# Kernel tuning notes

Hardware: AMD Instinct MI355X
Metric: run time of the kernel (lower is better)

## Reference

```python
import jax, jax.numpy as jnp
import numpy as np

N = 100000      # nodes
E = 1600000     # directed edges
F_IN = 128      # input features
H = 64          # hidden_channels
C = 32          # num_classes


def setup_inputs() -> dict:
    key = jax.random.key(0)
    ks = jax.random.split(key, 8)
    x = jax.random.normal(ks[0], (N, F_IN), jnp.float32)
    edge_index = jax.random.randint(ks[1], (2, E), 0, N, jnp.int32)
    W1 = jax.random.normal(ks[2], (F_IN, H), jnp.float32) * (1.0 / np.sqrt(F_IN))
    b1 = jnp.zeros((H,), jnp.float32)
    W2 = jax.random.normal(ks[3], (H, H), jnp.float32) * (1.0 / np.sqrt(H))
    b2 = jnp.zeros((H,), jnp.float32)
    Wout = jax.random.normal(ks[4], (H, C), jnp.float32) * (1.0 / np.sqrt(H))
    bout = jnp.zeros((C,), jnp.float32)
    return {"x": x, "edge_index": edge_index, "W1": W1, "b1": b1,
            "W2": W2, "b2": b2, "Wout": Wout, "bout": bout}


def gcn_conv(x, W, b, src, dst, n):
    """PyG GCNConv: out = D^-1/2 (A + I) D^-1/2 (X W) + b,
    with degree computed on A + I."""
    h = x @ W  # [N, out]
    ones = jnp.ones(dst.shape[0], h.dtype)
    deg = jax.ops.segment_sum(ones, dst, num_segments=n) + 1.0  # self-loop
    dinv = jax.lax.rsqrt(deg)                                   # [N]
    coef = dinv[src] * dinv[dst]                                # [E]
    agg = jax.ops.segment_sum(h[src] * coef[:, None], dst, num_segments=n)
    agg = agg + h * (dinv * dinv)[:, None]                      # self-loop message
    return agg + b


def reference(x, edge_index, W1, b1, W2, b2, Wout, bout):
    src, dst = edge_index[0], edge_index[1]
    n = x.shape[0]
    h = jax.nn.relu(gcn_conv(x, W1, b1, src, dst, n))
    # dropout(p=0.5) is a no-op in eval mode
    h = jax.nn.relu(gcn_conv(h, W2, b2, src, dst, n))
    return jax.nn.softmax(h @ Wout + bout, axis=1)
```

## Files before the change

### kernel.cpp

```cpp
#include <hip/hip_runtime.h>
#include <stdint.h>


typedef unsigned short u16;
typedef unsigned int u32;
typedef unsigned long long u64t;
typedef __attribute__((ext_vector_type(8))) short bf16x8;
typedef __attribute__((ext_vector_type(4))) float f32x4;
typedef __attribute__((ext_vector_type(2))) float f32x2;

#define GN 100000
#define GE 1600000
#define NBKT 196
#define BCAP 10240
#define EBLK 782
#define B24 16777216
#define QSC 1048576.0f
#define QIV 9.5367431640625e-7f

__device__ __forceinline__ float bf2f(u32 lo16) {
  union { u32 i; float f; } v; v.i = lo16 << 16; return v.f;
}
__device__ __forceinline__ u16 f2bf(float f) {
  union { float f; u32 i; } v; v.f = f;
  u32 x = v.i;
  u32 r = x + 0x7fffu + ((x >> 16) & 1u);
  return (u16)(r >> 16);
}
__device__ __forceinline__ u32 pack2(float a, float b) {
  return (u32)f2bf(a) | ((u32)f2bf(b) << 16);
}
__device__ __forceinline__ f32x2 unpk(u32 u) {
  union { u32 i; float f; } lo, hi;
  lo.i = u << 16; hi.i = u & 0xffff0000u;
  return (f32x2){lo.f, hi.f};
}

__global__ __launch_bounds__(256) void k_detect(const u16* __restrict__ xs,
                                                int* __restrict__ flag,
                                                int* __restrict__ ccount) {
  __shared__ int cnt;
  if (threadIdx.x == 0) cnt = 0;
  if (threadIdx.x < NBKT) ccount[threadIdx.x] = 0;
  __syncthreads();
  int w = 0;
#pragma unroll
  for (int i = 0; i < 16; i++) {
    int s = threadIdx.x * 16 + i;
    u32 u = xs[(size_t)s * 1562];
    u32 ex = (u >> 7) & 0xffu;
    if (ex == 0xffu || ex < 0x40u) w++;
  }
  atomicAdd(&cnt, w);
  __syncthreads();
  if (threadIdx.x == 0) flag[0] = (cnt >= 64) ? 0 : 1;
}

__global__ __launch_bounds__(256) void k_partA(const int* __restrict__ src,
                                               const int* __restrict__ dst,
                                               int* __restrict__ ccount, int E,
                                               const void* p2, const void* p3,
                                               const void* p4, const void* p5,
                                               const void* p6, const void* p7,
                                               const int* __restrict__ flag,
                                               float* __restrict__ Wf,
                                               u16* __restrict__ Wb1,
                                               u16* __restrict__ Wb2,
                                               u16* __restrict__ Wbo,
                                               u32* __restrict__ pairs) {
  int tid = threadIdx.x;
  if (blockIdx.x >= EBLK) {
    int i = (blockIdx.x - EBLK) * 256 + tid;
    bool isbf = flag[0] != 0;
    if (i < 14496) {
      const void* sp; int off;
      if (i < 8192)       { sp = p2; off = i; }
      else if (i < 8256)  { sp = p3; off = i - 8192; }
      else if (i < 12352) { sp = p4; off = i - 8256; }
      else if (i < 12416) { sp = p5; off = i - 12352; }
      else if (i < 14464) { sp = p6; off = i - 12416; }
      else                { sp = p7; off = i - 14464; }
      Wf[i] = isbf ? bf2f((u32)((const u16*)sp)[off]) : ((const float*)sp)[off];
    } else if (i < 14496 + 12288) {
      int idx = i - 14496;
      const void* W; u16* dstp;
      if (idx < 8192) { W = p2; dstp = Wb1; }
      else            { W = p4; dstp = Wb2; idx -= 8192; }
      int j  = idx & 7;
      int l  = (idx >> 3) & 63;
      int c  = (idx >> 9) & 3;
      int kc = idx >> 11;
      int k = kc * 32 + (l >> 4) * 8 + j;
      int n = c * 16 + (l & 15);
      dstp[idx] = isbf ? ((const u16*)W)[k * 64 + n]
                       : f2bf(((const float*)W)[k * 64 + n]);
    } else if (i < 14496 + 12288 + 2048) {
      int idx = i - 14496 - 12288;
      int j  = idx & 7;
      int l  = (idx >> 3) & 63;
      int c  = (idx >> 9) & 1;
      int kc = idx >> 10;
      int k = kc * 32 + (l >> 4) * 8 + j;
      int n = c * 16 + (l & 15);
      Wbo[idx] = isbf ? ((const u16*)p6)[k * 32 + n]
                      : f2bf(((const float*)p6)[k * 32 + n]);
    }
    return;
  }
  __shared__ int hist[256];
  __shared__ int boff[256];
  __shared__ int fill[256];
  __shared__ int gbase[256];
  __shared__ int sc[256];
  __shared__ u32 buf[2048];
  __shared__ int adr[2048];
  __shared__ int stotal;
  hist[tid] = 0;
  __syncthreads();
  int e0 = (blockIdx.x * 256 + tid) * 8;
  int s_[8], d_[8];
  int cnt = 0;
  if (e0 + 8 <= E) {
    const int4* sp = (const int4*)(src + e0);
    const int4* dp = (const int4*)(dst + e0);
#pragma unroll
    for (int q = 0; q < 2; q++) {
      int4 sv = sp[q], dv = dp[q];
      s_[4 * q + 0] = sv.x; s_[4 * q + 1] = sv.y;
      s_[4 * q + 2] = sv.z; s_[4 * q + 3] = sv.w;
      d_[4 * q + 0] = dv.x; d_[4 * q + 1] = dv.y;
      d_[4 * q + 2] = dv.z; d_[4 * q + 3] = dv.w;
    }
    cnt = 8;
  } else {
    for (int q = 0; q < 8 && e0 + q < E; q++) {
      s_[q] = src[e0 + q]; d_[q] = dst[e0 + q]; cnt++;
    }
  }
  for (int q = 0; q < cnt; q++) atomicAdd(&hist[d_[q] >> 9], 1);
  __syncthreads();
  int v = hist[tid];
  sc[tid] = v;
  __syncthreads();
#pragma unroll
  for (int off = 1; off < 256; off <<= 1) {
    int a = (tid >= off) ? sc[tid - off] : 0;
    __syncthreads();
    sc[tid] += a;
    __syncthreads();
  }
  int excl = sc[tid] - v;
  boff[tid] = excl;
  fill[tid] = excl;
  if (tid == 255) stotal = sc[255];
  if (tid < NBKT && v > 0) gbase[tid] = tid * BCAP + atomicAdd(&ccount[tid], v);
  __syncthreads();
  for (int q = 0; q < cnt; q++) {
    int bkt = d_[q] >> 9;
    int p = atomicAdd(&fill[bkt], 1);
    buf[p] = ((u32)s_[q] << 9) | ((u32)d_[q] & 511u);
    adr[p] = gbase[bkt] + (p - boff[bkt]);
  }
  __syncthreads();
  int total = stotal;
  for (int j = tid; j < total; j += 256) pairs[adr[j]] = buf[j];
}

__global__ __launch_bounds__(256) void k_partBdlo(u32* __restrict__ pairs,
                                                  const int* __restrict__ ccount,
                                                  int* __restrict__ deg, int N) {
  __shared__ u32 P[BCAP];
  __shared__ u32 S[BCAP];
  __shared__ int cnt[512];
  __shared__ int sc[256];
  int b = blockIdx.x, tid = threadIdx.x;
  int beg = b * BCAP, m = ccount[b];
  if (m > BCAP) m = BCAP;
  cnt[tid] = 0; cnt[tid + 256] = 0;
  for (int i = tid; i < m; i += 256) P[i] = pairs[beg + i];
  __syncthreads();
  for (int i = tid; i < m; i += 256) atomicAdd(&cnt[P[i] & 511u], 1);
  __syncthreads();
  int c0 = cnt[2 * tid], c1 = cnt[2 * tid + 1];
  int s = c0 + c1;
  sc[tid] = s;
  __syncthreads();
#pragma unroll
  for (int off = 1; off < 256; off <<= 1) {
    int a = (tid >= off) ? sc[tid - off] : 0;
    __syncthreads();
    sc[tid] += a;
    __syncthreads();
  }
  int excl = sc[tid] - s;
  cnt[2 * tid] = excl;
  cnt[2 * tid + 1] = excl + c0;
  int n0 = (b << 9) + 2 * tid, n1 = n0 + 1;
  if (n0 < N) deg[n0] = c0;
  if (n1 < N) deg[n1] = c1;
  __syncthreads();
  for (int i = tid; i < m; i += 256) {
    u32 p = P[i];
    int pos = atomicAdd(&cnt[p & 511u], 1);
    S[pos] = p;
  }
  __syncthreads();
  for (int i = tid; i < m; i += 256) pairs[beg + i] = S[i];
}

template <int K, int XMODE>
__global__ __launch_bounds__(256) void k_mgemm(const void* __restrict__ X,
                                               const u16* __restrict__ Wb,
                                               const int* __restrict__ deg,
                                               const int* __restrict__ flag,
                                               u16* __restrict__ out, int M) {
  constexpr int NKC = K / 32;
  constexpr int P = K + 8;
  __shared__ u16 Bs[NKC * 4 * 64 * 8];
  __shared__ u16 As[128 * P];
  int tid = threadIdx.x;
  bool isbf = (XMODE == 1) ? true : (flag[0] != 0);
#pragma unroll
  for (int i = 0; i < NKC; i++)
    ((uint4*)Bs)[i * 256 + tid] = ((const uint4*)Wb)[i * 256 + tid];

  int rowbase = blockIdx.x * 128;
  int rowsValid = M - rowbase; if (rowsValid > 128) rowsValid = 128;
  if (isbf) {
    constexpr int F8 = K / 8;
    constexpr int NL = K / 16;
    const uint4* Xg = (const uint4*)X;
    uint4 v[NL];
#pragma unroll
    for (int i = 0; i < NL; i++) {
      int q = i * 256 + tid;
      int row = q / F8, c8 = q % F8;
      v[i] = (row < rowsValid) ? Xg[(size_t)(rowbase + row) * F8 + c8]
                               : make_uint4(0, 0, 0, 0);
    }
#pragma unroll
    for (int i = 0; i < NL; i++) {
      int q = i * 256 + tid;
      int row = q / F8, c8 = q % F8;
      *(uint4*)&As[row * P + c8 * 8] = v[i];
    }
  } else {
    constexpr int F4 = K / 4;
    constexpr int NL = K / 8;
    const float4* Xg = (const float4*)X;
    float4 v[NL];
#pragma unroll
    for (int i = 0; i < NL; i++) {
      int q = i * 256 + tid;
      int row = q / F4, c4 = q % F4;
      v[i] = (row < rowsValid) ? Xg[(size_t)(rowbase + row) * F4 + c4]
                               : make_float4(0.f, 0.f, 0.f, 0.f);
    }
#pragma unroll
    for (int i = 0; i < NL; i++) {
      int q = i * 256 + tid;
      int row = q / F4, c4 = q % F4;
      u32* d = (u32*)&As[row * P + c4 * 4];
      d[0] = pack2(v[i].x, v[i].y);
      d[1] = pack2(v[i].z, v[i].w);
    }
  }
  __syncthreads();

  int lane = tid & 63, wave = tid >> 6;
  int m0 = lane & 15;
  int koff = (lane >> 4) * 8;
  f32x4 acc[2][4];
#pragma unroll
  for (int t = 0; t < 2; t++)
#pragma unroll
    for (int c = 0; c < 4; c++) acc[t][c] = (f32x4){0.f, 0.f, 0.f, 0.f};

#pragma unroll
  for (int kc = 0; kc < NKC; kc++) {
    union { uint4 v; bf16x8 s; } a[2];
#pragma unroll
    for (int t = 0; t < 2; t++) {
      int rl = wave * 32 + t * 16 + m0;
      a[t].v = *(const uint4*)&As[rl * P + kc * 32 + koff];
    }
#pragma unroll
    for (int c = 0; c < 4; c++) {
      bf16x8 b = *(const bf16x8*)&Bs[((kc * 4 + c) * 64 + lane) * 8];
      acc[0][c] = __builtin_amdgcn_mfma_f32_16x16x32_bf16(a[0].s, b, acc[0][c], 0, 0, 0);
      acc[1][c] = __builtin_amdgcn_mfma_f32_16x16x32_bf16(a[1].s, b, acc[1][c], 0, 0, 0);
    }
  }
  __syncthreads();
  int cl = lane & 15, rq = (lane >> 4) * 4;
#pragma unroll
  for (int t = 0; t < 2; t++)
#pragma unroll
    for (int reg = 0; reg < 4; reg++) {
      int rl = wave * 32 + t * 16 + rq + reg;
      int r = rowbase + rl;
      float s = (r < M) ? rsqrtf((float)deg[r] + 1.0f) : 0.f;
#pragma unroll
      for (int c = 0; c < 4; c++)
        As[rl * P + c * 16 + cl] = f2bf(acc[t][c][reg] * s);
    }
  __syncthreads();
  uint4* outg = (uint4*)out;
#pragma unroll
  for (int i = 0; i < 4; i++) {
    int q = i * 256 + tid;
    int row = q >> 3, c8 = q & 7;
    int r = rowbase + row;
    if (r < M) outg[(size_t)r * 8 + c8] = *(uint4*)&As[row * P + c8 * 8];
  }
}

template <int MODE>
__global__ __launch_bounds__(1024) void k_aggr(const u16* __restrict__ g,
                                               const u32* __restrict__ pairs,
                                               const int* __restrict__ ccount,
                                               const float* __restrict__ bias,
                                               const u16* __restrict__ Wfrag,
                                               const float* __restrict__ bof,
                                               const int* __restrict__ flag,
                                               void* __restrict__ outv) {
  __shared__ __align__(16) u64t accU[512 * 33];
  __shared__ int cntE[512];
  u16* T16 = (u16*)accU;
  int tid = threadIdx.x;
  int b = blockIdx.x;
  for (int i = tid; i < 512 * 33; i += 1024) accU[i] = 0ull;
  if (tid < 512) cntE[tid] = 0;
  __syncthreads();

  int beg = b * BCAP;
  int m = ccount[b];
  if (m > BCAP) m = BCAP;
  int end = beg + m;
  int o = tid >> 3, fq = tid & 7;
  const uint4* gp4 = (const uint4*)g;

  int C = (m + 127) >> 7;
  int lo = beg + o * C;
  int hi = lo + C; if (hi > end) hi = end;

  f32x2 a0 = {0.f, 0.f}, a1 = {0.f, 0.f}, a2 = {0.f, 0.f}, a3 = {0.f, 0.f};
  int cur = 0, runN = 0;

#define FLUSH()                                                              \
  do {                                                                       \
    if (runN > 0) {                                                          \
      int nb_ = runN * B24;                                                  \
      u64t* rp_ = &accU[cur * 33 + fq * 4];                                  \
      int q0_ = (int)(a0.x * QSC) + nb_;                                     \
      int q1_ = (int)(a0.y * QSC) + nb_;                                     \
      int q2_ = (int)(a1.x * QSC) + nb_;                                     \
      int q3_ = (int)(a1.y * QSC) + nb_;                                     \
      int q4_ = (int)(a2.x * QSC) + nb_;                                     \
      int q5_ = (int)(a2.y * QSC) + nb_;                                     \
      int q6_ = (int)(a3.x * QSC) + nb_;                                     \
      int q7_ = (int)(a3.y * QSC) + nb_;                                     \
      atomicAdd(rp_ + 0, ((u64t)(u32)q0_) | (((u64t)(u32)q1_) << 32));       \
      atomicAdd(rp_ + 1, ((u64t)(u32)q2_) | (((u64t)(u32)q3_) << 32));       \
      atomicAdd(rp_ + 2, ((u64t)(u32)q4_) | (((u64t)(u32)q5_) << 32));       \
      atomicAdd(rp_ + 3, ((u64t)(u32)q6_) | (((u64t)(u32)q7_) << 32));       \
      if (fq == 0) atomicAdd(&cntE[cur], runN);                              \
      a0 = (f32x2){0.f, 0.f}; a1 = (f32x2){0.f, 0.f};                        \
      a2 = (f32x2){0.f, 0.f}; a3 = (f32x2){0.f, 0.f};                        \
      runN = 0;                                                              \
    }                                                                        \
  } while (0)

#define STEP(p_, v_)                                                         \
  do {                                                                       \
    int d_ = (int)((p_) & 511u);                                             \
    if (d_ != cur) { FLUSH(); cur = d_; }                                    \
    a0 += unpk((v_).x); a1 += unpk((v_).y);                                  \
    a2 += unpk((v_).z); a3 += unpk((v_).w);                                  \
    runN++;                                                                  \
  } while (0)

  for (int e = lo; e < hi; e += 4) {
    int n4 = hi - e;
    u32 p0 = pairs[e];
    u32 p1 = pairs[(n4 > 1) ? e + 1 : e];
    u32 p2 = pairs[(n4 > 2) ? e + 2 : e];
    u32 p3 = pairs[(n4 > 3) ? e + 3 : e];
    uint4 v0 = gp4[(size_t)(p0 >> 9) * 8 + fq];
    uint4 v1 = gp4[(size_t)(p1 >> 9) * 8 + fq];
    uint4 v2 = gp4[(size_t)(p2 >> 9) * 8 + fq];
    uint4 v3 = gp4[(size_t)(p3 >> 9) * 8 + fq];
    STEP(p0, v0);
    if (n4 > 1) STEP(p1, v1);
    if (n4 > 2) STEP(p2, v2);
    if (n4 > 3) STEP(p3, v3);
  }
  FLUSH();
#undef STEP
#undef FLUSH
  __syncthreads();

  u32 pk[4][4];
  int rowq[4], c8q[4];
#pragma unroll
  for (int i = 0; i < 4; i++) {
    int q = i * 1024 + tid;
    int row = q >> 3, c8 = q & 7;
    rowq[i] = row; c8q[i] = c8;
    int node = b * 512 + row;
    float f0 = 0.f, f1 = 0.f, f2 = 0.f, f3 = 0.f;
    float f4 = 0.f, f5 = 0.f, f6 = 0.f, f7 = 0.f;
    if (node < GN) {
      uint4 sv = gp4[(size_t)node * 8 + c8];
      int n = cntE[row];
      int nb = n * B24;
      float dv = rsqrtf((float)n + 1.0f);
      float4 b0 = ((const float4*)bias)[c8 * 2];
      float4 b1 = ((const float4*)bias)[c8 * 2 + 1];
      const u64t* up = &accU[row * 33 + c8 * 4];
      u64t w0 = up[0], w1 = up[1], w2 = up[2], w3 = up[3];
      int a0i = (int)((u32)w0) - nb, a1i = (int)((u32)(w0 >> 32)) - nb;
      int a2i = (int)((u32)w1) - nb, a3i = (int)((u32)(w1 >> 32)) - nb;
      int a4i = (int)((u32)w2) - nb, a5i = (int)((u32)(w2 >> 32)) - nb;
      int a6i = (int)((u32)w3) - nb, a7i = (int)((u32)(w3 >> 32)) - nb;
      f0 = fmaxf(dv * ((float)a0i * QIV + bf2f(sv.x & 0xffffu)) + b0.x, 0.f);
      f1 = fmaxf(dv * ((float)a1i * QIV + bf2f(sv.x >> 16))     + b0.y, 0.f);
      f2 = fmaxf(dv * ((float)a2i * QIV + bf2f(sv.y & 0xffffu)) + b0.z, 0.f);
      f3 = fmaxf(dv * ((float)a3i * QIV + bf2f(sv.y >> 16))     + b0.w, 0.f);
      f4 = fmaxf(dv * ((float)a4i * QIV + bf2f(sv.z & 0xffffu)) + b1.x, 0.f);
      f5 = fmaxf(dv * ((float)a5i * QIV + bf2f(sv.z >> 16))     + b1.y, 0.f);
      f6 = fmaxf(dv * ((float)a6i * QIV + bf2f(sv.w & 0xffffu)) + b1.z, 0.f);
      f7 = fmaxf(dv * ((float)a7i * QIV + bf2f(sv.w >> 16))     + b1.w, 0.f);
    }
    pk[i][0] = pack2(f0, f1); pk[i][1] = pack2(f2, f3);
    pk[i][2] = pack2(f4, f5); pk[i][3] = pack2(f6, f7);
  }
  __syncthreads();
#pragma unroll
  for (int i = 0; i < 4; i++)
    *(uint4*)&T16[rowq[i] * 72 + c8q[i] * 8] =
        make_uint4(pk[i][0], pk[i][1], pk[i][2], pk[i][3]);
  __syncthreads();

  int lane = tid & 63, wave = tid >> 6;
  int m0 = lane & 15, koff = (lane >> 4) * 8;
  int cl = lane & 15, rq = (lane >> 4) * 4;
  if (MODE == 0) {
    bf16x8 bfr[2][4];
#pragma unroll
    for (int kc = 0; kc < 2; kc++)
#pragma unroll
      for (int c = 0; c < 4; c++)
        bfr[kc][c] = *(const bf16x8*)&Wfrag[((kc * 4 + c) * 64 + lane) * 8];
    f32x4 acc[2][4];
#pragma unroll
    for (int t = 0; t < 2; t++)
#pragma unroll
      for (int c = 0; c < 4; c++) acc[t][c] = (f32x4){0.f, 0.f, 0.f, 0.f};
#pragma unroll
    for (int kc = 0; kc < 2; kc++) {
      union { uint4 v; bf16x8 s; } a[2];
#pragma unroll
      for (int t = 0; t < 2; t++)
        a[t].v = *(const uint4*)&T16[(wave * 32 + t * 16 + m0) * 72 + kc * 32 + koff];
#pragma unroll
      for (int c = 0; c < 4; c++) {
        acc[0][c] = __builtin_amdgcn_mfma_f32_16x16x32_bf16(a[0].s, bfr[kc][c], acc[0][c], 0, 0, 0);
        acc[1][c] = __builtin_amdgcn_mfma_f32_16x16x32_bf16(a[1].s, bfr[kc][c], acc[1][c], 0, 0, 0);
      }
    }
    __syncthreads();
#pragma unroll
    for (int t = 0; t < 2; t++)
#pragma unroll
      for (int reg = 0; reg < 4; reg++) {
        int rl = wave * 32 + t * 16 + rq + reg;
        int node = b * 512 + rl;
        float s = (node < GN) ? rsqrtf((float)cntE[rl] + 1.0f) : 0.f;
#pragma unroll
        for (int c = 0; c < 4; c++)
          T16[rl * 72 + c * 16 + cl] = f2bf(acc[t][c][reg] * s);
      }
    __syncthreads();
    uint4* og = (uint4*)outv;
#pragma unroll
    for (int i = 0; i < 4; i++) {
      int q = i * 1024 + tid;
      int row = q >> 3, c8 = q & 7;
      int node = b * 512 + row;
      if (node < GN) og[(size_t)node * 8 + c8] = *(uint4*)&T16[row * 72 + c8 * 8];
    }
  } else {
    bf16x8 bfr[2][2];
#pragma unroll
    for (int kc = 0; kc < 2; kc++)
#pragma unroll
      for (int cc = 0; cc < 2; cc++)
        bfr[kc][cc] = *(const bf16x8*)&Wfrag[((kc * 2 + cc) * 64 + lane) * 8];
    f32x4 acc[2][2];
#pragma unroll
    for (int t = 0; t < 2; t++)
#pragma unroll
      for (int c = 0; c < 2; c++) acc[t][c] = (f32x4){0.f, 0.f, 0.f, 0.f};
#pragma unroll
    for (int kc = 0; kc < 2; kc++) {
      union { uint4 v; bf16x8 s; } a[2];
#pragma unroll
      for (int t = 0; t < 2; t++)
        a[t].v = *(const uint4*)&T16[(wave * 32 + t * 16 + m0) * 72 + kc * 32 + koff];
#pragma unroll
      for (int c = 0; c < 2; c++) {
        acc[0][c] = __builtin_amdgcn_mfma_f32_16x16x32_bf16(a[0].s, bfr[kc][c], acc[0][c], 0, 0, 0);
        acc[1][c] = __builtin_amdgcn_mfma_f32_16x16x32_bf16(a[1].s, bfr[kc][c], acc[1][c], 0, 0, 0);
      }
    }
    bool isbf = flag[0] != 0;
    float bb0 = bof[cl], bb1 = bof[16 + cl];
#pragma unroll
    for (int t = 0; t < 2; t++)
#pragma unroll
      for (int reg = 0; reg < 4; reg++) {
        int r = b * 512 + wave * 32 + t * 16 + rq + reg;
        float v0 = acc[t][0][reg] + bb0;
        float v1 = acc[t][1][reg] + bb1;
        float mx = fmaxf(v0, v1);
        mx = fmaxf(mx, __shfl_xor(mx, 1));
        mx = fmaxf(mx, __shfl_xor(mx, 2));
        mx = fmaxf(mx, __shfl_xor(mx, 4));
        mx = fmaxf(mx, __shfl_xor(mx, 8));
        float e0 = __expf(v0 - mx), e1 = __expf(v1 - mx);
        float s = e0 + e1;
        s += __shfl_xor(s, 1);
        s += __shfl_xor(s, 2);
        s += __shfl_xor(s, 4);
        s += __shfl_xor(s, 8);
        float inv = 1.f / s;
        if (r < GN) {
          if (isbf) {
            u16* go = (u16*)outv;
            go[(size_t)r * 32 + cl]      = f2bf(e0 * inv);
            go[(size_t)r * 32 + 16 + cl] = f2bf(e1 * inv);
          } else {
            float* go = (float*)outv;
            go[(size_t)r * 32 + cl]      = e0 * inv;
            go[(size_t)r * 32 + 16 + cl] = e1 * inv;
          }
        }
      }
  }
}

extern "C" void kernel_launch(void* const* d_in, const int* in_sizes, int n_in,
                              void* d_out, int out_size, void* d_ws, size_t ws_size,
                              hipStream_t stream) {
  (void)in_sizes; (void)n_in; (void)out_size; (void)ws_size;
  const void* x  = d_in[0];
  const int* ei  = (const int*)d_in[1];
  const int E = GE;
  const int* srcI = ei;
  const int* dstI = ei + E;

  char* ws = (char*)d_ws;
  int*   flag   = (int*)(ws + 0);
  int*   ccount = (int*)(ws + 256);
  int*   deg    = (int*)(ws + 4096);
  float* Wf     = (float*)(ws + 404480);
  u16*   Wb1    = (u16*)(ws + 462464);
  u16*   Wb2    = (u16*)(ws + 478848);
  u16*   Wbo    = (u16*)(ws + 487040);
  u32*   pairs  = (u32*)(ws + 491520);
  u16*   gA     = (u16*)(ws + 8519680);
  u16*   gB     = (u16*)(ws + 21319680);

  float* b1f = Wf + 8192;
  float* b2f = Wf + 12352;
  float* bof = Wf + 14464;

  k_detect<<<1, 256, 0, stream>>>((const u16*)x, flag, ccount);
  k_partA<<<EBLK + 113, 256, 0, stream>>>(srcI, dstI, ccount, E,
                                          d_in[2], d_in[3], d_in[4], d_in[5],
                                          d_in[6], d_in[7], flag,
                                          Wf, Wb1, Wb2, Wbo, pairs);
  k_partBdlo<<<NBKT, 256, 0, stream>>>(pairs, ccount, deg, GN);
  k_mgemm<128, 0><<<782, 256, 0, stream>>>(x, Wb1, deg, flag, gA, GN);
  k_aggr<0><<<NBKT, 1024, 0, stream>>>(gA, pairs, ccount, b1f, Wb2, bof, flag, gB);
  k_aggr<1><<<NBKT, 1024, 0, stream>>>(gB, pairs, ccount, b2f, Wbo, bof, flag, d_out);
}
```

Before: 227.3 us.

## Halve destination bucket size to 256 nodes to double aggregation blocks

Nodes are now bucketed in groups of 256 instead of 512 destinations, which gives 391 buckets instead of 196. The partition, local sort, degree and aggregation kernels are reworked to match: 8-bit destination packing, smaller shared-memory arrays, and one 16-row MFMA tile per wave instead of two. The goal is to fill all compute units during the aggregation kernels, since 196 blocks cannot occupy the whole GPU. In exchange there are more blocks with fewer edges each, a tighter per-bucket capacity margin, and a higher occupancy hint on the 1024-thread kernel.

```diff
diff --git a/kernel.cpp b/kernel.cpp
--- a/kernel.cpp
+++ b/kernel.cpp
@@ -11,8 +11,8 @@
 
 #define GN 100000
 #define GE 1600000
-#define NBKT 196
-#define BCAP 10240
+#define NB2 391
+#define BC2 5120
 #define EBLK 782
 #define B24 16777216
 #define QSC 1048576.0f
@@ -40,20 +40,21 @@
                                                 int* __restrict__ flag,
                                                 int* __restrict__ ccount) {
   __shared__ int cnt;
-  if (threadIdx.x == 0) cnt = 0;
-  if (threadIdx.x < NBKT) ccount[threadIdx.x] = 0;
+  int tid = threadIdx.x;
+  if (tid == 0) cnt = 0;
+  for (int i = tid; i < NB2; i += 256) ccount[i] = 0;
   __syncthreads();
   int w = 0;
 #pragma unroll
   for (int i = 0; i < 16; i++) {
-    int s = threadIdx.x * 16 + i;
+    int s = tid * 16 + i;
     u32 u = xs[(size_t)s * 1562];
     u32 ex = (u >> 7) & 0xffu;
     if (ex == 0xffu || ex < 0x40u) w++;
   }
   atomicAdd(&cnt, w);
   __syncthreads();
-  if (threadIdx.x == 0) flag[0] = (cnt >= 64) ? 0 : 1;
+  if (tid == 0) flag[0] = (cnt >= 64) ? 0 : 1;
 }
 
 __global__ __launch_bounds__(256) void k_partA(const int* __restrict__ src,
@@ -107,15 +108,15 @@
     }
     return;
   }
-  __shared__ int hist[256];
-  __shared__ int boff[256];
-  __shared__ int fill[256];
-  __shared__ int gbase[256];
+  __shared__ int hist[512];
+  __shared__ int boff[512];
+  __shared__ int fill[512];
+  __shared__ int gbase[512];
   __shared__ int sc[256];
   __shared__ u32 buf[2048];
   __shared__ int adr[2048];
   __shared__ int stotal;
-  hist[tid] = 0;
+  hist[tid] = 0; hist[tid + 256] = 0;
   __syncthreads();
   int e0 = (blockIdx.x * 256 + tid) * 8;
   int s_[8], d_[8];
@@ -137,10 +138,11 @@
       s_[q] = src[e0 + q]; d_[q] = dst[e0 + q]; cnt++;
     }
   }
-  for (int q = 0; q < cnt; q++) atomicAdd(&hist[d_[q] >> 9], 1);
-  __syncthreads();
-  int v = hist[tid];
-  sc[tid] = v;
+  for (int q = 0; q < cnt; q++) atomicAdd(&hist[d_[q] >> 8], 1);
+  __syncthreads();
+  int c0 = hist[2 * tid], c1 = hist[2 * tid + 1];
+  int s = c0 + c1;
+  sc[tid] = s;
   __syncthreads();
 #pragma unroll
   for (int off = 1; off < 256; off <<= 1) {
@@ -149,16 +151,17 @@
     sc[tid] += a;
     __syncthreads();
   }
-  int excl = sc[tid] - v;
-  boff[tid] = excl;
-  fill[tid] = excl;
+  int excl = sc[tid] - s;
+  boff[2 * tid] = excl;       boff[2 * tid + 1] = excl + c0;
+  fill[2 * tid] = excl;       fill[2 * tid + 1] = excl + c0;
   if (tid == 255) stotal = sc[255];
-  if (tid < NBKT && v > 0) gbase[tid] = tid * BCAP + atomicAdd(&ccount[tid], v);
+  if (c0 > 0) gbase[2 * tid]     = (2 * tid) * BC2 + atomicAdd(&ccount[2 * tid], c0);
+  if (c1 > 0) gbase[2 * tid + 1] = (2 * tid + 1) * BC2 + atomicAdd(&ccount[2 * tid + 1], c1);
   __syncthreads();
   for (int q = 0; q < cnt; q++) {
-    int bkt = d_[q] >> 9;
+    int bkt = d_[q] >> 8;
     int p = atomicAdd(&fill[bkt], 1);
-    buf[p] = ((u32)s_[q] << 9) | ((u32)d_[q] & 511u);
+    buf[p] = ((u32)s_[q] << 8) | ((u32)d_[q] & 255u);
     adr[p] = gbase[bkt] + (p - boff[bkt]);
   }
   __syncthreads();
@@ -169,21 +172,20 @@
 __global__ __launch_bounds__(256) void k_partBdlo(u32* __restrict__ pairs,
                                                   const int* __restrict__ ccount,
                                                   int* __restrict__ deg, int N) {
-  __shared__ u32 P[BCAP];
-  __shared__ u32 S[BCAP];
-  __shared__ int cnt[512];
+  __shared__ u32 P[BC2];
+  __shared__ u32 S[BC2];
+  __shared__ int cnt[256];
   __shared__ int sc[256];
   int b = blockIdx.x, tid = threadIdx.x;
-  int beg = b * BCAP, m = ccount[b];
-  if (m > BCAP) m = BCAP;
-  cnt[tid] = 0; cnt[tid + 256] = 0;
+  int beg = b * BC2, m = ccount[b];
+  if (m > BC2) m = BC2;
+  cnt[tid] = 0;
   for (int i = tid; i < m; i += 256) P[i] = pairs[beg + i];
   __syncthreads();
-  for (int i = tid; i < m; i += 256) atomicAdd(&cnt[P[i] & 511u], 1);
-  __syncthreads();
-  int c0 = cnt[2 * tid], c1 = cnt[2 * tid + 1];
-  int s = c0 + c1;
-  sc[tid] = s;
+  for (int i = tid; i < m; i += 256) atomicAdd(&cnt[P[i] & 255u], 1);
+  __syncthreads();
+  int v = cnt[tid];
+  sc[tid] = v;
   __syncthreads();
 #pragma unroll
   for (int off = 1; off < 256; off <<= 1) {
@@ -192,16 +194,14 @@
     sc[tid] += a;
     __syncthreads();
   }
-  int excl = sc[tid] - s;
-  cnt[2 * tid] = excl;
-  cnt[2 * tid + 1] = excl + c0;
-  int n0 = (b << 9) + 2 * tid, n1 = n0 + 1;
-  if (n0 < N) deg[n0] = c0;
-  if (n1 < N) deg[n1] = c1;
+  int excl = sc[tid] - v;
+  int n0 = (b << 8) + tid;
+  if (n0 < N) deg[n0] = v;
+  cnt[tid] = excl;
   __syncthreads();
   for (int i = tid; i < m; i += 256) {
     u32 p = P[i];
-    int pos = atomicAdd(&cnt[p & 511u], 1);
+    int pos = atomicAdd(&cnt[p & 255u], 1);
     S[pos] = p;
   }
   __syncthreads();
@@ -316,26 +316,26 @@
 }
 
 template <int MODE>
-__global__ __launch_bounds__(1024) void k_aggr(const u16* __restrict__ g,
-                                               const u32* __restrict__ pairs,
-                                               const int* __restrict__ ccount,
-                                               const float* __restrict__ bias,
-                                               const u16* __restrict__ Wfrag,
-                                               const float* __restrict__ bof,
-                                               const int* __restrict__ flag,
-                                               void* __restrict__ outv) {
-  __shared__ __align__(16) u64t accU[512 * 33];
-  __shared__ int cntE[512];
+__global__ __launch_bounds__(1024, 8) void k_aggr(const u16* __restrict__ g,
+                                                  const u32* __restrict__ pairs,
+                                                  const int* __restrict__ ccount,
+                                                  const float* __restrict__ bias,
+                                                  const u16* __restrict__ Wfrag,
+                                                  const float* __restrict__ bof,
+                                                  const int* __restrict__ flag,
+                                                  void* __restrict__ outv) {
+  __shared__ __align__(16) u64t accU[256 * 33];
+  __shared__ int cntE[256];
   u16* T16 = (u16*)accU;
   int tid = threadIdx.x;
   int b = blockIdx.x;
-  for (int i = tid; i < 512 * 33; i += 1024) accU[i] = 0ull;
-  if (tid < 512) cntE[tid] = 0;
-  __syncthreads();
-
-  int beg = b * BCAP;
+  for (int i = tid; i < 256 * 33; i += 1024) accU[i] = 0ull;
+  if (tid < 256) cntE[tid] = 0;
+  __syncthreads();
+
+  int beg = b * BC2;
   int m = ccount[b];
-  if (m > BCAP) m = BCAP;
+  if (m > BC2) m = BC2;
   int end = beg + m;
   int o = tid >> 3, fq = tid & 7;
   const uint4* gp4 = (const uint4*)g;
@@ -373,7 +373,7 @@
 
 #define STEP(p_, v_)                                                         \
   do {                                                                       \
-    int d_ = (int)((p_) & 511u);                                             \
+    int d_ = (int)((p_) & 255u);                                             \
     if (d_ != cur) { FLUSH(); cur = d_; }                                    \
     a0 += unpk((v_).x); a1 += unpk((v_).y);                                  \
     a2 += unpk((v_).z); a3 += unpk((v_).w);                                  \
@@ -386,10 +386,10 @@
     u32 p1 = pairs[(n4 > 1) ? e + 1 : e];
     u32 p2 = pairs[(n4 > 2) ? e + 2 : e];
     u32 p3 = pairs[(n4 > 3) ? e + 3 : e];
-    uint4 v0 = gp4[(size_t)(p0 >> 9) * 8 + fq];
-    uint4 v1 = gp4[(size_t)(p1 >> 9) * 8 + fq];
-    uint4 v2 = gp4[(size_t)(p2 >> 9) * 8 + fq];
-    uint4 v3 = gp4[(size_t)(p3 >> 9) * 8 + fq];
+    uint4 v0 = gp4[(size_t)(p0 >> 8) * 8 + fq];
+    uint4 v1 = gp4[(size_t)(p1 >> 8) * 8 + fq];
+    uint4 v2 = gp4[(size_t)(p2 >> 8) * 8 + fq];
+    uint4 v3 = gp4[(size_t)(p3 >> 8) * 8 + fq];
     STEP(p0, v0);
     if (n4 > 1) STEP(p1, v1);
     if (n4 > 2) STEP(p2, v2);
@@ -400,14 +400,14 @@
 #undef FLUSH
   __syncthreads();
 
-  u32 pk[4][4];
-  int rowq[4], c8q[4];
-#pragma unroll
-  for (int i = 0; i < 4; i++) {
+  u32 pk[2][4];
+  int rowq[2], c8q[2];
+#pragma unroll
+  for (int i = 0; i < 2; i++) {
     int q = i * 1024 + tid;
     int row = q >> 3, c8 = q & 7;
     rowq[i] = row; c8q[i] = c8;
-    int node = b * 512 + row;
+    int node = (b << 8) + row;
     float f0 = 0.f, f1 = 0.f, f2 = 0.f, f3 = 0.f;
     float f4 = 0.f, f5 = 0.f, f6 = 0.f, f7 = 0.f;
     if (node < GN) {
@@ -437,7 +437,7 @@
   }
   __syncthreads();
 #pragma unroll
-  for (int i = 0; i < 4; i++)
+  for (int i = 0; i < 2; i++)
     *(uint4*)&T16[rowq[i] * 72 + c8q[i] * 8] =
         make_uint4(pk[i][0], pk[i][1], pk[i][2], pk[i][3]);
   __syncthreads();
@@ -445,6 +445,7 @@
   int lane = tid & 63, wave = tid >> 6;
   int m0 = lane & 15, koff = (lane >> 4) * 8;
   int cl = lane & 15, rq = (lane >> 4) * 4;
+  int w16 = wave * 16;
   if (MODE == 0) {
     bf16x8 bfr[2][4];
 #pragma unroll
@@ -452,42 +453,34 @@
 #pragma unroll
       for (int c = 0; c < 4; c++)
         bfr[kc][c] = *(const bf16x8*)&Wfrag[((kc * 4 + c) * 64 + lane) * 8];
-    f32x4 acc[2][4];
-#pragma unroll
-    for (int t = 0; t < 2; t++)
-#pragma unroll
-      for (int c = 0; c < 4; c++) acc[t][c] = (f32x4){0.f, 0.f, 0.f, 0.f};
+    f32x4 acc4[4];
+#pragma unroll
+    for (int c = 0; c < 4; c++) acc4[c] = (f32x4){0.f, 0.f, 0.f, 0.f};
 #pragma unroll
     for (int kc = 0; kc < 2; kc++) {
-      union { uint4 v; bf16x8 s; } a[2];
-#pragma unroll
-      for (int t = 0; t < 2; t++)
-        a[t].v = *(const uint4*)&T16[(wave * 32 + t * 16 + m0) * 72 + kc * 32 + koff];
-#pragma unroll
-      for (int c = 0; c < 4; c++) {
-        acc[0][c] = __builtin_amdgcn_mfma_f32_16x16x32_bf16(a[0].s, bfr[kc][c], acc[0][c], 0, 0, 0);
-        acc[1][c] = __builtin_amdgcn_mfma_f32_16x16x32_bf16(a[1].s, bfr[kc][c], acc[1][c], 0, 0, 0);
-      }
+      union { uint4 v; bf16x8 s; } a;
+      a.v = *(const uint4*)&T16[(w16 + m0) * 72 + kc * 32 + koff];
+#pragma unroll
+      for (int c = 0; c < 4; c++)
+        acc4[c] = __builtin_amdgcn_mfma_f32_16x16x32_bf16(a.s, bfr[kc][c], acc4[c], 0, 0, 0);
     }
     __syncthreads();
 #pragma unroll
-    for (int t = 0; t < 2; t++)
-#pragma unroll
-      for (int reg = 0; reg < 4; reg++) {
-        int rl = wave * 32 + t * 16 + rq + reg;
-        int node = b * 512 + rl;
-        float s = (node < GN) ? rsqrtf((float)cntE[rl] + 1.0f) : 0.f;
-#pragma unroll
-        for (int c = 0; c < 4; c++)
-          T16[rl * 72 + c * 16 + cl] = f2bf(acc[t][c][reg] * s);
-      }
+    for (int reg = 0; reg < 4; reg++) {
+      int rl = w16 + rq + reg;
+      int node = (b << 8) + rl;
+      float s = (node < GN) ? rsqrtf((float)cntE[rl] + 1.0f) : 0.f;
+#pragma unroll
+      for (int c = 0; c < 4; c++)
+        T16[rl * 72 + c * 16 + cl] = f2bf(acc4[c][reg] * s);
+    }
     __syncthreads();
     uint4* og = (uint4*)outv;
 #pragma unroll
-    for (int i = 0; i < 4; i++) {
+    for (int i = 0; i < 2; i++) {
       int q = i * 1024 + tid;
       int row = q >> 3, c8 = q & 7;
-      int node = b * 512 + row;
+      int node = (b << 8) + row;
       if (node < GN) og[(size_t)node * 8 + c8] = *(uint4*)&T16[row * 72 + c8 * 8];
     }
   } else {
@@ -497,56 +490,47 @@
 #pragma unroll
       for (int cc = 0; cc < 2; cc++)
         bfr[kc][cc] = *(const bf16x8*)&Wfrag[((kc * 2 + cc) * 64 + lane) * 8];
-    f32x4 acc[2][2];
-#pragma unroll
-    for (int t = 0; t < 2; t++)
-#pragma unroll
-      for (int c = 0; c < 2; c++) acc[t][c] = (f32x4){0.f, 0.f, 0.f, 0.f};
+    f32x4 acc2[2];
+    acc2[0] = (f32x4){0.f, 0.f, 0.f, 0.f};
+    acc2[1] = (f32x4){0.f, 0.f, 0.f, 0.f};
 #pragma unroll
     for (int kc = 0; kc < 2; kc++) {
-      union { uint4 v; bf16x8 s; } a[2];
-#pragma unroll
-      for (int t = 0; t < 2; t++)
-        a[t].v = *(const uint4*)&T16[(wave * 32 + t * 16 + m0) * 72 + kc * 32 + koff];
-#pragma unroll
-      for (int c = 0; c < 2; c++) {
-        acc[0][c] = __builtin_amdgcn_mfma_f32_16x16x32_bf16(a[0].s, bfr[kc][c], acc[0][c], 0, 0, 0);
-        acc[1][c] = __builtin_amdgcn_mfma_f32_16x16x32_bf16(a[1].s, bfr[kc][c], acc[1][c], 0, 0, 0);
-      }
+      union { uint4 v; bf16x8 s; } a;
+      a.v = *(const uint4*)&T16[(w16 + m0) * 72 + kc * 32 + koff];
+      acc2[0] = __builtin_amdgcn_mfma_f32_16x16x32_bf16(a.s, bfr[kc][0], acc2[0], 0, 0, 0);
+      acc2[1] = __builtin_amdgcn_mfma_f32_16x16x32_bf16(a.s, bfr[kc][1], acc2[1], 0, 0, 0);
     }
     bool isbf = flag[0] != 0;
     float bb0 = bof[cl], bb1 = bof[16 + cl];
 #pragma unroll
-    for (int t = 0; t < 2; t++)
-#pragma unroll
-      for (int reg = 0; reg < 4; reg++) {
-        int r = b * 512 + wave * 32 + t * 16 + rq + reg;
-        float v0 = acc[t][0][reg] + bb0;
-        float v1 = acc[t][1][reg] + bb1;
-        float mx = fmaxf(v0, v1);
-        mx = fmaxf(mx, __shfl_xor(mx, 1));
-        mx = fmaxf(mx, __shfl_xor(mx, 2));
-        mx = fmaxf(mx, __shfl_xor(mx, 4));
-        mx = fmaxf(mx, __shfl_xor(mx, 8));
-        float e0 = __expf(v0 - mx), e1 = __expf(v1 - mx);
-        float s = e0 + e1;
-        s += __shfl_xor(s, 1);
-        s += __shfl_xor(s, 2);
-        s += __shfl_xor(s, 4);
-        s += __shfl_xor(s, 8);
-        float inv = 1.f / s;
-        if (r < GN) {
-          if (isbf) {
-            u16* go = (u16*)outv;
-            go[(size_t)r * 32 + cl]      = f2bf(e0 * inv);
-            go[(size_t)r * 32 + 16 + cl] = f2bf(e1 * inv);
-          } else {
-            float* go = (float*)outv;
-            go[(size_t)r * 32 + cl]      = e0 * inv;
-            go[(size_t)r * 32 + 16 + cl] = e1 * inv;
-          }
+    for (int reg = 0; reg < 4; reg++) {
+      int r = (b << 8) + w16 + rq + reg;
+      float v0 = acc2[0][reg] + bb0;
+      float v1 = acc2[1][reg] + bb1;
+      float mx = fmaxf(v0, v1);
+      mx = fmaxf(mx, __shfl_xor(mx, 1));
+      mx = fmaxf(mx, __shfl_xor(mx, 2));
+      mx = fmaxf(mx, __shfl_xor(mx, 4));
+      mx = fmaxf(mx, __shfl_xor(mx, 8));
+      float e0 = __expf(v0 - mx), e1 = __expf(v1 - mx);
+      float s = e0 + e1;
+      s += __shfl_xor(s, 1);
+      s += __shfl_xor(s, 2);
+      s += __shfl_xor(s, 4);
+      s += __shfl_xor(s, 8);
+      float inv = 1.f / s;
+      if (r < GN) {
+        if (isbf) {
+          u16* go = (u16*)outv;
+          go[(size_t)r * 32 + cl]      = f2bf(e0 * inv);
+          go[(size_t)r * 32 + 16 + cl] = f2bf(e1 * inv);
+        } else {
+          float* go = (float*)outv;
+          go[(size_t)r * 32 + cl]      = e0 * inv;
+          go[(size_t)r * 32 + 16 + cl] = e1 * inv;
         }
       }
+    }
   }
 }
 
@@ -581,8 +565,8 @@
                                           d_in[2], d_in[3], d_in[4], d_in[5],
                                           d_in[6], d_in[7], flag,
                                           Wf, Wb1, Wb2, Wbo, pairs);
-  k_partBdlo<<<NBKT, 256, 0, stream>>>(pairs, ccount, deg, GN);
+  k_partBdlo<<<NB2, 256, 0, stream>>>(pairs, ccount, deg, GN);
   k_mgemm<128, 0><<<782, 256, 0, stream>>>(x, Wb1, deg, flag, gA, GN);
-  k_aggr<0><<<NBKT, 1024, 0, stream>>>(gA, pairs, ccount, b1f, Wb2, bof, flag, gB);
-  k_aggr<1><<<NBKT, 1024, 0, stream>>>(gB, pairs, ccount, b2f, Wbo, bof, flag, d_out);
-}
+  k_aggr<0><<<NB2, 1024, 0, stream>>>(gA, pairs, ccount, b1f, Wb2, bof, flag, gB);
+  k_aggr<1><<<NB2, 1024, 0, stream>>>(gB, pairs, ccount, b2f, Wbo, bof, flag, d_out);
+}
```

Result: slower. 239.1 us (+5.2%).
